# Kernel tuning notes

Hardware: AMD Instinct MI355X
Metric: run time of the kernel (lower is better)

## Reference

```python
import jax, jax.numpy as jnp
import numpy as np

PRE_HEIGHT = 96
PRE_WIDTH = 128


def setup_inputs() -> dict:
    key = jax.random.key(0)
    B, K, H, W = 32, 64, 96, 128
    x = jax.random.normal(key, (B, K, H, W), dtype=jnp.float32)
    return {"combined_hm_preds": x, "batch_size": B, "num_of_kp": K}


def reference(combined_hm_preds, batch_size, num_of_kp):
    B, K, H, W = combined_hm_preds.shape
    # nn.Softmax() with no dim on a 4D tensor -> softmax over dim=1 (channels)
    map_val_all = jax.nn.softmax(combined_hm_preds, axis=1)
    # zeta[b,k] = sum over spatial of the channel-softmaxed map
    get_zeta = map_val_all.sum(axis=(2, 3))  # [B, K]
    js = jnp.arange(W, dtype=map_val_all.dtype)
    iis = jnp.arange(H, dtype=map_val_all.dtype)
    # per-channel weighted coordinate sums
    Sx = jnp.einsum('bkij,j->bk', map_val_all, js)  # [B, K]
    Sy = jnp.einsum('bkij,i->bk', map_val_all, iis)  # [B, K]
    # faithful to the original: accumulators are never reset across k or b,
    # so each keypoint uses the inclusive cumulative sum in flattened (b,k) order
    cum_x = jnp.cumsum(Sx.reshape(-1)).reshape(B, K)
    cum_y = jnp.cumsum(Sy.reshape(-1)).reshape(B, K)
    kx = jnp.round(cum_x / get_zeta)
    ky = jnp.round(cum_y / get_zeta)
    # out-of-range clamp to the image center, as in the original
    kx = jnp.where((kx > PRE_WIDTH) | (kx < 0), PRE_WIDTH * 0.5, kx)
    ky = jnp.where((ky > PRE_HEIGHT) | (ky < 0), PRE_HEIGHT * 0.5, ky)
    keypoint = jnp.stack([kx, ky], axis=-1)  # [B, K, 2]
    return (map_val_all, keypoint, get_zeta)
```

## Files before the change

### kernel.cpp

```cpp
#include <hip/hip_runtime.h>
#include <math.h>

#define BB 32
#define KK 64
#define HH 96
#define WW 128
#define HW (HH*WW)
#define MAP_SIZE (BB*KK*HW)
#define NBK (BB*KK)
#define NT  (HW/256)
#define SST 259

__global__ __launch_bounds__(256, 2) void fused_k(const float* __restrict__ x,
                                                  float* __restrict__ out,
                                                  double* __restrict__ sxyz) {
    __shared__ float sm[KK][SST];

    int blk  = blockIdx.x;
    int b    = blk / NT;
    int tile = blk - b * NT;
    int t    = threadIdx.x;
    size_t base = (size_t)b * (KK * HW) + (size_t)tile * 256 + t;

    float den = 0.f;
    #pragma unroll
    for (int k = 0; k < KK; ++k) {
        float e = __expf(x[base + (size_t)k * HW]);
        sm[k][t] = e;
        den += e;
    }
    float inv = 1.f / den;

    #pragma unroll
    for (int k = 0; k < KK; ++k) {
        float m = sm[k][t] * inv;
        __builtin_nontemporal_store(m, &out[base + (size_t)k * HW]);
        sm[k][t] = m;
    }
    __syncthreads();

    int k = t >> 2;
    int q = t & 3;
    const float gy_base = (float)(tile * 2);
    float z = 0.f, sx = 0.f, sy = 0.f;
    #pragma unroll
    for (int j = 0; j < 16; ++j) {
        int p0 = q * 4 + j * 16;
        float m0 = sm[k][p0 + 0];
        float m1 = sm[k][p0 + 1];
        float m2 = sm[k][p0 + 2];
        float m3 = sm[k][p0 + 3];
        float s = (m0 + m1) + (m2 + m3);
        z  += s;
        sx += fmaf(s, (float)(p0 & (WW - 1)), fmaf(3.f, m3, fmaf(2.f, m2, m1)));
        sy += s * (gy_base + (float)(p0 >> 7));
    }

    z  += __shfl_xor(z,  1, 64);  z  += __shfl_xor(z,  2, 64);
    sx += __shfl_xor(sx, 1, 64);  sx += __shfl_xor(sx, 2, 64);
    sy += __shfl_xor(sy, 1, 64);  sy += __shfl_xor(sy, 2, 64);
    if (q == 0) {
        int bk = b * KK + k;
        atomicAdd(&sxyz[bk * 3 + 0], (double)sx);
        atomicAdd(&sxyz[bk * 3 + 1], (double)sy);
        atomicAdd(&sxyz[bk * 3 + 2], (double)z);
    }
}

__global__ __launch_bounds__(256) void keypoint_k(const double* __restrict__ sxyz,
                                                  float* __restrict__ kp,
                                                  float* __restrict__ zeta) {
    const int PT = NBK / 256;
    int t = threadIdx.x;
    int lane = t & 63, wid = t >> 6;

    double vx[PT], vy[PT], vz[PT];
    double cx = 0.0, cy = 0.0;
    #pragma unroll
    for (int e = 0; e < PT; ++e) {
        int idx = t * PT + e;
        cx += sxyz[idx * 3 + 0]; vx[e] = cx;
        cy += sxyz[idx * 3 + 1]; vy[e] = cy;
        vz[e] = sxyz[idx * 3 + 2];
    }
    double tx = cx, ty = cy;
    for (int off = 1; off < 64; off <<= 1) {
        double ax = __shfl_up(tx, off, 64);
        double ay = __shfl_up(ty, off, 64);
        if (lane >= off) { tx += ax; ty += ay; }
    }
    __shared__ double wxs[4], wys[4];
    if (lane == 63) { wxs[wid] = tx; wys[wid] = ty; }
    __syncthreads();
    double offx = tx - cx, offy = ty - cy;
    for (int w2 = 0; w2 < wid; ++w2) { offx += wxs[w2]; offy += wys[w2]; }

    #pragma unroll
    for (int e = 0; e < PT; ++e) {
        int idx = t * PT + e;
        double zz = vz[e];
        double kx = rint((vx[e] + offx) / zz);
        double ky = rint((vy[e] + offy) / zz);
        float fkx = (float)kx, fky = (float)ky;
        if (fkx > 128.0f || fkx < 0.0f) fkx = 64.0f;
        if (fky > 96.0f  || fky < 0.0f) fky = 48.0f;
        kp[idx * 2 + 0] = fkx;
        kp[idx * 2 + 1] = fky;
        zeta[idx] = (float)zz;
    }
}

extern "C" void kernel_launch(void* const* d_in, const int* in_sizes, int n_in,
                              void* d_out, int out_size, void* d_ws, size_t ws_size,
                              hipStream_t stream) {
    const float* x = (const float*)d_in[0];
    float* out  = (float*)d_out;
    float* map  = out;
    float* kp   = out + MAP_SIZE;
    float* zeta = out + MAP_SIZE + NBK * 2;
    double* sxyz = (double*)d_ws;

    hipMemsetAsync(d_ws, 0, (size_t)NBK * 3 * sizeof(double), stream);
    fused_k   <<< BB * NT, 256, 0, stream >>> (x, map, sxyz);
    keypoint_k<<< 1,       256, 0, stream >>> (sxyz, kp, zeta);
}
```

Measured before the change: 186.3 us.

## Use 64-thread blocks with per-thread channel reduction over 64-pixel tiles

Shrinks each block to one wavefront handling 64 pixels, so there are four times as many blocks. The per-channel spatial reduction becomes a serial loop in which each thread owns one channel, which removes the cross-lane shuffles. The cost is four times as many double-precision atomic adds into the shared accumulators, which raises contention on them.

Result: slower. 196.1 us (+5.2%).

```diff
diff --git a/kernel.cpp b/kernel.cpp
--- a/kernel.cpp
+++ b/kernel.cpp
@@ -8,19 +8,20 @@
 #define HW (HH*WW)
 #define MAP_SIZE (BB*KK*HW)
 #define NBK (BB*KK)
-#define NT  (HW/256)
-#define SST 259
+#define TK 64
+#define NTB (HW/TK)
+#define NBLK (BB*NTB)
 
-__global__ __launch_bounds__(256, 2) void fused_k(const float* __restrict__ x,
-                                                  float* __restrict__ out,
-                                                  double* __restrict__ sxyz) {
-    __shared__ float sm[KK][SST];
+__global__ __launch_bounds__(64, 2) void fused_k(const float* __restrict__ x,
+                                                 float* __restrict__ out,
+                                                 double* __restrict__ sxyz) {
+    __shared__ float sm[KK][65];
 
     int blk  = blockIdx.x;
-    int b    = blk / NT;
-    int tile = blk - b * NT;
+    int b    = blk / NTB;
+    int tile = blk - b * NTB;
     int t    = threadIdx.x;
-    size_t base = (size_t)b * (KK * HW) + (size_t)tile * 256 + t;
+    size_t base = (size_t)b * (KK * HW) + (size_t)tile * TK + t;
 
     float den = 0.f;
     #pragma unroll
@@ -39,32 +40,19 @@
     }
     __syncthreads();
 
-    int k = t >> 2;
-    int q = t & 3;
-    const float gy_base = (float)(tile * 2);
-    float z = 0.f, sx = 0.f, sy = 0.f;
+    float z = 0.f, sxl = 0.f;
     #pragma unroll
-    for (int j = 0; j < 16; ++j) {
-        int p0 = q * 4 + j * 16;
-        float m0 = sm[k][p0 + 0];
-        float m1 = sm[k][p0 + 1];
-        float m2 = sm[k][p0 + 2];
-        float m3 = sm[k][p0 + 3];
-        float s = (m0 + m1) + (m2 + m3);
-        z  += s;
-        sx += fmaf(s, (float)(p0 & (WW - 1)), fmaf(3.f, m3, fmaf(2.f, m2, m1)));
-        sy += s * (gy_base + (float)(p0 >> 7));
+    for (int j = 0; j < 64; ++j) {
+        float m = sm[t][j];
+        z   += m;
+        sxl  = fmaf(m, (float)j, sxl);
     }
-
-    z  += __shfl_xor(z,  1, 64);  z  += __shfl_xor(z,  2, 64);
-    sx += __shfl_xor(sx, 1, 64);  sx += __shfl_xor(sx, 2, 64);
-    sy += __shfl_xor(sy, 1, 64);  sy += __shfl_xor(sy, 2, 64);
-    if (q == 0) {
-        int bk = b * KK + k;
-        atomicAdd(&sxyz[bk * 3 + 0], (double)sx);
-        atomicAdd(&sxyz[bk * 3 + 1], (double)sy);
-        atomicAdd(&sxyz[bk * 3 + 2], (double)z);
-    }
+    float gxb = (float)((tile & 1) << 6);
+    float gy  = (float)(tile >> 1);
+    int bk = b * KK + t;
+    atomicAdd(&sxyz[bk * 3 + 0], (double)fmaf(gxb, z, sxl));
+    atomicAdd(&sxyz[bk * 3 + 1], (double)(gy * z));
+    atomicAdd(&sxyz[bk * 3 + 2], (double)z);
 }
 
 __global__ __launch_bounds__(256) void keypoint_k(const double* __restrict__ sxyz,
@@ -121,6 +109,6 @@
     double* sxyz = (double*)d_ws;
 
     hipMemsetAsync(d_ws, 0, (size_t)NBK * 3 * sizeof(double), stream);
-    fused_k   <<< BB * NT, 256, 0, stream >>> (x, map, sxyz);
-    keypoint_k<<< 1,       256, 0, stream >>> (sxyz, kp, zeta);
+    fused_k   <<< NBLK, TK, 0, stream >>> (x, map, sxyz);
+    keypoint_k<<< 1,    256, 0, stream >>> (sxyz, kp, zeta);
 }
```

## Split softmax into separate denominator pass and map/reduction pass

Applied to the files above, without the earlier changes.

Computes the per-pixel softmax denominator in a dedicated kernel with batched independent loads, storing the reciprocal to workspace. The main kernel then recomputes exp from x, scales by the stored reciprocal, and performs the spatial reductions. This targets the latency of the long dependent load/exp chain in the fused kernel, at the cost of reading the input twice and an extra launch.

Measured after the change: 199.5 us. 7.1% more time.

```diff
diff --git a/kernel.cpp b/kernel.cpp
--- a/kernel.cpp
+++ b/kernel.cpp
@@ -9,11 +9,35 @@
 #define MAP_SIZE (BB*KK*HW)
 #define NBK (BB*KK)
 #define NT  (HW/256)
+#define NPX (BB*HW)
 #define SST 259
 
-__global__ __launch_bounds__(256, 2) void fused_k(const float* __restrict__ x,
-                                                  float* __restrict__ out,
-                                                  double* __restrict__ sxyz) {
+__global__ __launch_bounds__(256) void den_k(const float* __restrict__ x,
+                                             float* __restrict__ invd) {
+    int blk  = blockIdx.x;
+    int b    = blk / NT;
+    int tile = blk - b * NT;
+    int t    = threadIdx.x;
+    size_t base = (size_t)b * (KK * HW) + (size_t)tile * 256 + t;
+
+    float den = 0.f;
+    #pragma unroll
+    for (int c = 0; c < 4; ++c) {
+        float v[16];
+        #pragma unroll
+        for (int j = 0; j < 16; ++j)
+            v[j] = x[base + (size_t)(c * 16 + j) * HW];
+        #pragma unroll
+        for (int j = 0; j < 16; ++j)
+            den += __expf(v[j]);
+    }
+    invd[(size_t)blk * 256 + t] = 1.f / den;
+}
+
+__global__ __launch_bounds__(256, 2) void map_k(const float* __restrict__ x,
+                                                const float* __restrict__ invd,
+                                                float* __restrict__ out,
+                                                double* __restrict__ sxyz) {
     __shared__ float sm[KK][SST];
 
     int blk  = blockIdx.x;
@@ -22,18 +46,11 @@
     int t    = threadIdx.x;
     size_t base = (size_t)b * (KK * HW) + (size_t)tile * 256 + t;
 
-    float den = 0.f;
-    #pragma unroll
-    for (int k = 0; k < KK; ++k) {
-        float e = __expf(x[base + (size_t)k * HW]);
-        sm[k][t] = e;
-        den += e;
-    }
-    float inv = 1.f / den;
+    float inv = invd[(size_t)blk * 256 + t];
 
     #pragma unroll
     for (int k = 0; k < KK; ++k) {
-        float m = sm[k][t] * inv;
+        float m = __expf(x[base + (size_t)k * HW]) * inv;
         __builtin_nontemporal_store(m, &out[base + (size_t)k * HW]);
         sm[k][t] = m;
     }
@@ -119,8 +136,10 @@
     float* kp   = out + MAP_SIZE;
     float* zeta = out + MAP_SIZE + NBK * 2;
     double* sxyz = (double*)d_ws;
+    float*  invd = (float*)((char*)d_ws + 65536);
 
     hipMemsetAsync(d_ws, 0, (size_t)NBK * 3 * sizeof(double), stream);
-    fused_k   <<< BB * NT, 256, 0, stream >>> (x, map, sxyz);
+    den_k     <<< BB * NT, 256, 0, stream >>> (x, invd);
+    map_k     <<< BB * NT, 256, 0, stream >>> (x, invd, map, sxyz);
     keypoint_k<<< 1,       256, 0, stream >>> (sxyz, kp, zeta);
 }
```
